# Optimization experiments

Hardware: AMD Instinct MI355X
Metric: run time of the kernel (lower is better)

Reference implementation:

```python
import jax, jax.numpy as jnp
import numpy as np

IN_FEATURES = 4096
OUT_FEATURES = 4096
BATCH = 4096
MASK_DENSITY = 0.05  # typical power-grid neighborhood sparsity


def setup_inputs() -> dict:
    key = jax.random.key(0)
    k_x, k_w, k_b, k_m = jax.random.split(key, 4)
    x = jax.random.normal(k_x, (BATCH, IN_FEATURES), dtype=jnp.float32)
    # kaiming_uniform_(a=sqrt(5)) -> uniform(-bound, bound), bound = sqrt(6/((1+5)*fan_in)) = 1/sqrt(fan_in)
    w_bound = 1.0 / np.sqrt(IN_FEATURES)
    weight = jax.random.uniform(k_w, (OUT_FEATURES, IN_FEATURES), dtype=jnp.float32,
                                minval=-w_bound, maxval=w_bound)
    bias = jax.random.uniform(k_b, (OUT_FEATURES,), dtype=jnp.float32,
                              minval=-w_bound, maxval=w_bound)
    # fixed binary neighborhood filter (non-trainable), int-valued {0,1} as in the torch module
    myFilter = (jax.random.uniform(k_m, (OUT_FEATURES, IN_FEATURES)) < MASK_DENSITY).astype(jnp.float32)
    return {"x": x, "weight": weight, "bias": bias, "myFilter": myFilter}


def reference(x, weight, bias, myFilter):
    # F.linear(input, weight * myFilter, bias): y = x @ (W * M)^T + b
    masked_w = weight * myFilter                      # [out, in]
    return jnp.einsum('bi,oi->bo', x, masked_w) + bias  # [batch, out]
```

## Files before the change

kernel.cpp:

```cpp
#include <hip/hip_runtime.h>
#include <hip/hip_bf16.h>
#include <stdint.h>

#define IN_F   4096
#define OUT_F  4096
#define BATCH  4096

typedef __bf16 bf16x8_t __attribute__((ext_vector_type(8)));
typedef float  f32x4_t  __attribute__((ext_vector_type(4)));

#define AS_GLOBAL(p) ((const __attribute__((address_space(1))) void*)(p))
#define AS_LDS(p)    ((__attribute__((address_space(3))) void*)(p))

__device__ __forceinline__ unsigned short f32_to_bf16_rne(float f) {
    union { float f; uint32_t u; } v; v.f = f;
    uint32_t u = v.u;
    u += 0x7FFFu + ((u >> 16) & 1u);
    return (unsigned short)(u >> 16);
}

__global__ __launch_bounds__(256)
void convert_kernel(const float* __restrict__ x,
                    const float* __restrict__ w,
                    const float* __restrict__ m,
                    unsigned short* __restrict__ xb,
                    unsigned short* __restrict__ wb) {
    const int64_t i = (int64_t)blockIdx.x * 256 + threadIdx.x;
    float4 xv = ((const float4*)x)[i];
    float4 wv = ((const float4*)w)[i];
    float4 mv = ((const float4*)m)[i];
    ushort4 xo, wo;
    xo.x = f32_to_bf16_rne(xv.x);
    xo.y = f32_to_bf16_rne(xv.y);
    xo.z = f32_to_bf16_rne(xv.z);
    xo.w = f32_to_bf16_rne(xv.w);
    wo.x = f32_to_bf16_rne(wv.x * mv.x);
    wo.y = f32_to_bf16_rne(wv.y * mv.y);
    wo.z = f32_to_bf16_rne(wv.z * mv.z);
    wo.w = f32_to_bf16_rne(wv.w * mv.w);
    ((ushort4*)xb)[i] = xo;
    ((ushort4*)wb)[i] = wo;
}

#define BM 128
#define BN 128
#define BK 64

__global__ __launch_bounds__(256)
void gemm_bt_bias_kernel(const unsigned short* __restrict__ A,
                         const unsigned short* __restrict__ B,
                         const float* __restrict__ bias,
                         float* __restrict__ C) {
    __shared__ __align__(16) unsigned short sA[BM * BK];
    __shared__ __align__(16) unsigned short sB[BN * BK];

    const int t    = threadIdx.x;
    const int wv   = t >> 6;
    const int lane = t & 63;
    const int quad = lane >> 4;
    const int l16  = lane & 15;

    const int bm = blockIdx.y * BM;
    const int bn = blockIdx.x * BN;

    const int wr = wv >> 1;
    const int wc = wv & 1;

    const int srow = t >> 3;
    const int scol = 8 * ((t & 7) ^ ((t >> 3) & 7));
    const unsigned short* gA = A + (int64_t)(bm + srow) * IN_F + scol;
    const unsigned short* gB = B + (int64_t)(bn + srow) * IN_F + scol;

    f32x4_t acc[4][4];
#pragma unroll
    for (int mi = 0; mi < 4; ++mi)
#pragma unroll
        for (int ni = 0; ni < 4; ++ni)
            acc[mi][ni] = (f32x4_t){0.f, 0.f, 0.f, 0.f};

    for (int k0 = 0; k0 < IN_F; k0 += BK) {
        __syncthreads();
#pragma unroll
        for (int r = 0; r < 4; ++r) {
            __builtin_amdgcn_global_load_lds(
                AS_GLOBAL(gA + (int64_t)r * 32 * IN_F + k0),
                AS_LDS((char*)sA + r * 4096 + wv * 1024 + (lane * 16)), 16, 0, 0);
            __builtin_amdgcn_global_load_lds(
                AS_GLOBAL(gB + (int64_t)r * 32 * IN_F + k0),
                AS_LDS((char*)sB + r * 4096 + wv * 1024 + (lane * 16)), 16, 0, 0);
        }
        __syncthreads();

#pragma unroll
        for (int ks = 0; ks < 2; ++ks) {
            bf16x8_t af[4], bf[4];
#pragma unroll
            for (int mi = 0; mi < 4; ++mi) {
                const int row = wr * 64 + mi * 16 + l16;
                const int ch  = (ks * 4 + quad) ^ (row & 7);
                af[mi] = *(const bf16x8_t*)(sA + row * BK + ch * 8);
            }
#pragma unroll
            for (int ni = 0; ni < 4; ++ni) {
                const int row = wc * 64 + ni * 16 + l16;
                const int ch  = (ks * 4 + quad) ^ (row & 7);
                bf[ni] = *(const bf16x8_t*)(sB + row * BK + ch * 8);
            }
#pragma unroll
            for (int mi = 0; mi < 4; ++mi)
#pragma unroll
                for (int ni = 0; ni < 4; ++ni)
                    acc[mi][ni] = __builtin_amdgcn_mfma_f32_16x16x32_bf16(
                        af[mi], bf[ni], acc[mi][ni], 0, 0, 0);
        }
    }

    float bv[4];
#pragma unroll
    for (int ni = 0; ni < 4; ++ni)
        bv[ni] = bias[bn + wc * 64 + ni * 16 + l16];

#pragma unroll
    for (int mi = 0; mi < 4; ++mi) {
        const int row0 = bm + wr * 64 + mi * 16 + quad * 4;
#pragma unroll
        for (int ni = 0; ni < 4; ++ni) {
            const int col = bn + wc * 64 + ni * 16 + l16;
#pragma unroll
            for (int reg = 0; reg < 4; ++reg)
                C[(int64_t)(row0 + reg) * OUT_F + col] = acc[mi][ni][reg] + bv[ni];
        }
    }
}

__global__ void fallback_gemm_kernel(const float* __restrict__ x,
                                     const float* __restrict__ w,
                                     const float* __restrict__ bias,
                                     const float* __restrict__ m,
                                     float* __restrict__ y) {
    __shared__ float sx[16][17];
    __shared__ float sw[16][17];
    const int tx = threadIdx.x, ty = threadIdx.y;
    const int row = blockIdx.y * 16 + ty;
    const int col = blockIdx.x * 16 + tx;
    float acc = 0.f;
    for (int k0 = 0; k0 < IN_F; k0 += 16) {
        sx[ty][tx] = x[(int64_t)row * IN_F + k0 + tx];
        const int64_t widx = (int64_t)(blockIdx.x * 16 + ty) * IN_F + k0 + tx;
        sw[ty][tx] = w[widx] * m[widx];
        __syncthreads();
#pragma unroll
        for (int kk = 0; kk < 16; ++kk)
            acc += sx[ty][kk] * sw[tx][kk];
        __syncthreads();
    }
    y[(int64_t)row * OUT_F + col] = acc + bias[col];
}

extern "C" void kernel_launch(void* const* d_in, const int* in_sizes, int n_in,
                              void* d_out, int out_size, void* d_ws, size_t ws_size,
                              hipStream_t stream) {
    const float* x    = (const float*)d_in[0];
    const float* w    = (const float*)d_in[1];
    const float* bias = (const float*)d_in[2];
    const float* m    = (const float*)d_in[3];
    float* y = (float*)d_out;

    const size_t need = (size_t)2 * (size_t)OUT_F * (size_t)IN_F * sizeof(unsigned short);

    if (ws_size >= need) {
        unsigned short* xb = (unsigned short*)d_ws;
        unsigned short* wb = xb + (size_t)BATCH * IN_F;

        convert_kernel<<<16384, 256, 0, stream>>>(x, w, m, xb, wb);

        dim3 grid(OUT_F / BN, BATCH / BM);
        gemm_bt_bias_kernel<<<grid, 256, 0, stream>>>(xb, wb, bias, y);
    } else {
        dim3 grid(OUT_F / 16, BATCH / 16);
        dim3 block(16, 16);
        fallback_gemm_kernel<<<grid, block, 0, stream>>>(x, w, bias, m, y);
    }
}
```

Before: 341.8 us.

## Enlarge GEMM tile to 256x128 and overlap next-tile loads with MFMA

The GEMM block tile grows from 128x128 to 256x128, so each wave now holds 8x4 accumulators, which raises data reuse per loaded B fragment. The main loop is restructured so the first k-half is computed, the second k-half fragments are read into registers, and then the next tile's global-to-LDS loads are issued before the second half's MFMAs run, overlapping load latency with compute. The convert kernel processes two vectors per thread with nontemporal loads and half the grid. Risks are higher register pressure (128 accumulator floats plus 12 fragments), lower occupancy, and a smaller grid of 512 blocks for 256 CUs.

```diff
diff --git a/kernel.cpp b/kernel.cpp
--- a/kernel.cpp
+++ b/kernel.cpp
@@ -8,6 +8,8 @@
 
 typedef __bf16 bf16x8_t __attribute__((ext_vector_type(8)));
 typedef float  f32x4_t  __attribute__((ext_vector_type(4)));
+typedef float  f32x4v   __attribute__((ext_vector_type(4)));
+typedef unsigned short u16x4v __attribute__((ext_vector_type(4)));
 
 #define AS_GLOBAL(p) ((const __attribute__((address_space(1))) void*)(p))
 #define AS_LDS(p)    ((__attribute__((address_space(3))) void*)(p))
@@ -25,24 +27,28 @@
                     const float* __restrict__ m,
                     unsigned short* __restrict__ xb,
                     unsigned short* __restrict__ wb) {
-    const int64_t i = (int64_t)blockIdx.x * 256 + threadIdx.x;
-    float4 xv = ((const float4*)x)[i];
-    float4 wv = ((const float4*)w)[i];
-    float4 mv = ((const float4*)m)[i];
-    ushort4 xo, wo;
-    xo.x = f32_to_bf16_rne(xv.x);
-    xo.y = f32_to_bf16_rne(xv.y);
-    xo.z = f32_to_bf16_rne(xv.z);
-    xo.w = f32_to_bf16_rne(xv.w);
-    wo.x = f32_to_bf16_rne(wv.x * mv.x);
-    wo.y = f32_to_bf16_rne(wv.y * mv.y);
-    wo.z = f32_to_bf16_rne(wv.z * mv.z);
-    wo.w = f32_to_bf16_rne(wv.w * mv.w);
-    ((ushort4*)xb)[i] = xo;
-    ((ushort4*)wb)[i] = wo;
-}
-
-#define BM 128
+    const int64_t i0 = (int64_t)blockIdx.x * 512 + threadIdx.x;
+#pragma unroll
+    for (int u = 0; u < 2; ++u) {
+        const int64_t i = i0 + u * 256;
+        f32x4v xv = __builtin_nontemporal_load(&((const f32x4v*)x)[i]);
+        f32x4v wv = __builtin_nontemporal_load(&((const f32x4v*)w)[i]);
+        f32x4v mv = __builtin_nontemporal_load(&((const f32x4v*)m)[i]);
+        u16x4v xo, wo;
+        xo.x = f32_to_bf16_rne(xv.x);
+        xo.y = f32_to_bf16_rne(xv.y);
+        xo.z = f32_to_bf16_rne(xv.z);
+        xo.w = f32_to_bf16_rne(xv.w);
+        wo.x = f32_to_bf16_rne(wv.x * mv.x);
+        wo.y = f32_to_bf16_rne(wv.y * mv.y);
+        wo.z = f32_to_bf16_rne(wv.z * mv.z);
+        wo.w = f32_to_bf16_rne(wv.w * mv.w);
+        ((u16x4v*)xb)[i] = xo;
+        ((u16x4v*)wb)[i] = wo;
+    }
+}
+
+#define BM 256
 #define BN 128
 #define BK 64
 
@@ -71,48 +77,71 @@
     const unsigned short* gA = A + (int64_t)(bm + srow) * IN_F + scol;
     const unsigned short* gB = B + (int64_t)(bn + srow) * IN_F + scol;
 
-    f32x4_t acc[4][4];
-#pragma unroll
-    for (int mi = 0; mi < 4; ++mi)
+#define ISSUE_TILE(k0)                                                        \
+    do {                                                                      \
+        _Pragma("unroll")                                                     \
+        for (int r = 0; r < 8; ++r)                                           \
+            __builtin_amdgcn_global_load_lds(                                 \
+                AS_GLOBAL(gA + (int64_t)r * 32 * IN_F + (k0)),                \
+                AS_LDS((char*)sA + r * 4096 + wv * 1024 + lane * 16), 16, 0, 0); \
+        _Pragma("unroll")                                                     \
+        for (int r = 0; r < 4; ++r)                                           \
+            __builtin_amdgcn_global_load_lds(                                 \
+                AS_GLOBAL(gB + (int64_t)r * 32 * IN_F + (k0)),                \
+                AS_LDS((char*)sB + r * 4096 + wv * 1024 + lane * 16), 16, 0, 0); \
+    } while (0)
+
+    f32x4_t acc[8][4];
+#pragma unroll
+    for (int mi = 0; mi < 8; ++mi)
 #pragma unroll
         for (int ni = 0; ni < 4; ++ni)
             acc[mi][ni] = (f32x4_t){0.f, 0.f, 0.f, 0.f};
 
+    ISSUE_TILE(0);
+
     for (int k0 = 0; k0 < IN_F; k0 += BK) {
         __syncthreads();
-#pragma unroll
-        for (int r = 0; r < 4; ++r) {
-            __builtin_amdgcn_global_load_lds(
-                AS_GLOBAL(gA + (int64_t)r * 32 * IN_F + k0),
-                AS_LDS((char*)sA + r * 4096 + wv * 1024 + (lane * 16)), 16, 0, 0);
-            __builtin_amdgcn_global_load_lds(
-                AS_GLOBAL(gB + (int64_t)r * 32 * IN_F + k0),
-                AS_LDS((char*)sB + r * 4096 + wv * 1024 + (lane * 16)), 16, 0, 0);
-        }
-        __syncthreads();
-
-#pragma unroll
-        for (int ks = 0; ks < 2; ++ks) {
-            bf16x8_t af[4], bf[4];
-#pragma unroll
-            for (int mi = 0; mi < 4; ++mi) {
-                const int row = wr * 64 + mi * 16 + l16;
-                const int ch  = (ks * 4 + quad) ^ (row & 7);
-                af[mi] = *(const bf16x8_t*)(sA + row * BK + ch * 8);
-            }
-#pragma unroll
-            for (int ni = 0; ni < 4; ++ni) {
-                const int row = wc * 64 + ni * 16 + l16;
-                const int ch  = (ks * 4 + quad) ^ (row & 7);
-                bf[ni] = *(const bf16x8_t*)(sB + row * BK + ch * 8);
-            }
-#pragma unroll
-            for (int mi = 0; mi < 4; ++mi)
-#pragma unroll
-                for (int ni = 0; ni < 4; ++ni)
-                    acc[mi][ni] = __builtin_amdgcn_mfma_f32_16x16x32_bf16(
-                        af[mi], bf[ni], acc[mi][ni], 0, 0, 0);
-        }
+
+        bf16x8_t bf0[4];
+#pragma unroll
+        for (int ni = 0; ni < 4; ++ni) {
+            const int row = wc * 64 + ni * 16 + l16;
+            bf0[ni] = *(const bf16x8_t*)(sB + row * BK + (quad ^ (row & 7)) * 8);
+        }
+#pragma unroll
+        for (int mi = 0; mi < 8; ++mi) {
+            const int row = wr * 128 + mi * 16 + l16;
+            bf16x8_t af = *(const bf16x8_t*)(sA + row * BK + (quad ^ (row & 7)) * 8);
+#pragma unroll
+            for (int ni = 0; ni < 4; ++ni)
+                acc[mi][ni] = __builtin_amdgcn_mfma_f32_16x16x32_bf16(
+                    af, bf0[ni], acc[mi][ni], 0, 0, 0);
+        }
+
+        bf16x8_t bf1[4], af1[8];
+#pragma unroll
+        for (int ni = 0; ni < 4; ++ni) {
+            const int row = wc * 64 + ni * 16 + l16;
+            bf1[ni] = *(const bf16x8_t*)(sB + row * BK + ((4 + quad) ^ (row & 7)) * 8);
+        }
+#pragma unroll
+        for (int mi = 0; mi < 8; ++mi) {
+            const int row = wr * 128 + mi * 16 + l16;
+            af1[mi] = *(const bf16x8_t*)(sA + row * BK + ((4 + quad) ^ (row & 7)) * 8);
+        }
+
+        __syncthreads();
+
+        if (k0 + BK < IN_F)
+            ISSUE_TILE(k0 + BK);
+
+#pragma unroll
+        for (int mi = 0; mi < 8; ++mi)
+#pragma unroll
+            for (int ni = 0; ni < 4; ++ni)
+                acc[mi][ni] = __builtin_amdgcn_mfma_f32_16x16x32_bf16(
+                    af1[mi], bf1[ni], acc[mi][ni], 0, 0, 0);
     }
 
     float bv[4];
@@ -121,8 +150,8 @@
         bv[ni] = bias[bn + wc * 64 + ni * 16 + l16];
 
 #pragma unroll
-    for (int mi = 0; mi < 4; ++mi) {
-        const int row0 = bm + wr * 64 + mi * 16 + quad * 4;
+    for (int mi = 0; mi < 8; ++mi) {
+        const int row0 = bm + wr * 128 + mi * 16 + quad * 4;
 #pragma unroll
         for (int ni = 0; ni < 4; ++ni) {
             const int col = bn + wc * 64 + ni * 16 + l16;
@@ -131,6 +160,7 @@
                 C[(int64_t)(row0 + reg) * OUT_F + col] = acc[mi][ni][reg] + bv[ni];
         }
     }
+#undef ISSUE_TILE
 }
 
 __global__ void fallback_gemm_kernel(const float* __restrict__ x,
@@ -172,7 +202,7 @@
         unsigned short* xb = (unsigned short*)d_ws;
         unsigned short* wb = xb + (size_t)BATCH * IN_F;
 
-        convert_kernel<<<16384, 256, 0, stream>>>(x, w, m, xb, wb);
+        convert_kernel<<<8192, 256, 0, stream>>>(x, w, m, xb, wb);
 
         dim3 grid(OUT_F / BN, BATCH / BM);
         gemm_bt_bias_kernel<<<grid, 256, 0, stream>>>(xb, wb, bias, y);
```

Result: slower. 384.1 us (+12.4%).

## Double-buffer GEMM LDS tiles and unroll nontemporal convert kernel

Applied to the files above, without the earlier changes.

The GEMM now keeps two LDS buffers per operand. It issues the direct global-to-LDS loads for the next K tile before computing on the current tile, which drops one barrier per iteration and aims to hide global load latency behind MFMA work. The convert kernel handles two float4 groups per thread with nontemporal loads and launches half as many blocks, to cut streaming overhead. This doubles LDS use per block, which can lower occupancy. The overlap also depends on the compiler not inserting a full vmcnt wait before the LDS reads.

```diff
diff --git a/kernel.cpp b/kernel.cpp
--- a/kernel.cpp
+++ b/kernel.cpp
@@ -8,6 +8,8 @@
 
 typedef __bf16 bf16x8_t __attribute__((ext_vector_type(8)));
 typedef float  f32x4_t  __attribute__((ext_vector_type(4)));
+typedef float  f32x4v   __attribute__((ext_vector_type(4)));
+typedef unsigned short u16x4v __attribute__((ext_vector_type(4)));
 
 #define AS_GLOBAL(p) ((const __attribute__((address_space(1))) void*)(p))
 #define AS_LDS(p)    ((__attribute__((address_space(3))) void*)(p))
@@ -25,21 +27,25 @@
                     const float* __restrict__ m,
                     unsigned short* __restrict__ xb,
                     unsigned short* __restrict__ wb) {
-    const int64_t i = (int64_t)blockIdx.x * 256 + threadIdx.x;
-    float4 xv = ((const float4*)x)[i];
-    float4 wv = ((const float4*)w)[i];
-    float4 mv = ((const float4*)m)[i];
-    ushort4 xo, wo;
-    xo.x = f32_to_bf16_rne(xv.x);
-    xo.y = f32_to_bf16_rne(xv.y);
-    xo.z = f32_to_bf16_rne(xv.z);
-    xo.w = f32_to_bf16_rne(xv.w);
-    wo.x = f32_to_bf16_rne(wv.x * mv.x);
-    wo.y = f32_to_bf16_rne(wv.y * mv.y);
-    wo.z = f32_to_bf16_rne(wv.z * mv.z);
-    wo.w = f32_to_bf16_rne(wv.w * mv.w);
-    ((ushort4*)xb)[i] = xo;
-    ((ushort4*)wb)[i] = wo;
+    const int64_t i0 = (int64_t)blockIdx.x * 512 + threadIdx.x;
+#pragma unroll
+    for (int u = 0; u < 2; ++u) {
+        const int64_t i = i0 + u * 256;
+        f32x4v xv = __builtin_nontemporal_load(&((const f32x4v*)x)[i]);
+        f32x4v wv = __builtin_nontemporal_load(&((const f32x4v*)w)[i]);
+        f32x4v mv = __builtin_nontemporal_load(&((const f32x4v*)m)[i]);
+        u16x4v xo, wo;
+        xo.x = f32_to_bf16_rne(xv.x);
+        xo.y = f32_to_bf16_rne(xv.y);
+        xo.z = f32_to_bf16_rne(xv.z);
+        xo.w = f32_to_bf16_rne(xv.w);
+        wo.x = f32_to_bf16_rne(wv.x * mv.x);
+        wo.y = f32_to_bf16_rne(wv.y * mv.y);
+        wo.z = f32_to_bf16_rne(wv.z * mv.z);
+        wo.w = f32_to_bf16_rne(wv.w * mv.w);
+        ((u16x4v*)xb)[i] = xo;
+        ((u16x4v*)wb)[i] = wo;
+    }
 }
 
 #define BM 128
@@ -51,8 +57,8 @@
                          const unsigned short* __restrict__ B,
                          const float* __restrict__ bias,
                          float* __restrict__ C) {
-    __shared__ __align__(16) unsigned short sA[BM * BK];
-    __shared__ __align__(16) unsigned short sB[BN * BK];
+    __shared__ __align__(16) unsigned short sA[2][BM * BK];
+    __shared__ __align__(16) unsigned short sB[2][BN * BK];
 
     const int t    = threadIdx.x;
     const int wv   = t >> 6;
@@ -71,6 +77,19 @@
     const unsigned short* gA = A + (int64_t)(bm + srow) * IN_F + scol;
     const unsigned short* gB = B + (int64_t)(bn + srow) * IN_F + scol;
 
+#define ISSUE_TILE(buf, k0)                                                   \
+    do {                                                                      \
+        _Pragma("unroll")                                                     \
+        for (int r = 0; r < 4; ++r) {                                         \
+            __builtin_amdgcn_global_load_lds(                                 \
+                AS_GLOBAL(gA + (int64_t)r * 32 * IN_F + (k0)),                \
+                AS_LDS((char*)sA[buf] + r * 4096 + wv * 1024 + lane * 16), 16, 0, 0); \
+            __builtin_amdgcn_global_load_lds(                                 \
+                AS_GLOBAL(gB + (int64_t)r * 32 * IN_F + (k0)),                \
+                AS_LDS((char*)sB[buf] + r * 4096 + wv * 1024 + lane * 16), 16, 0, 0); \
+        }                                                                     \
+    } while (0)
+
     f32x4_t acc[4][4];
 #pragma unroll
     for (int mi = 0; mi < 4; ++mi)
@@ -78,18 +97,17 @@
         for (int ni = 0; ni < 4; ++ni)
             acc[mi][ni] = (f32x4_t){0.f, 0.f, 0.f, 0.f};
 
-    for (int k0 = 0; k0 < IN_F; k0 += BK) {
+    ISSUE_TILE(0, 0);
+
+    int buf = 0;
+    for (int k0 = 0; k0 < IN_F; k0 += BK, buf ^= 1) {
         __syncthreads();
-#pragma unroll
-        for (int r = 0; r < 4; ++r) {
-            __builtin_amdgcn_global_load_lds(
-                AS_GLOBAL(gA + (int64_t)r * 32 * IN_F + k0),
-                AS_LDS((char*)sA + r * 4096 + wv * 1024 + (lane * 16)), 16, 0, 0);
-            __builtin_amdgcn_global_load_lds(
-                AS_GLOBAL(gB + (int64_t)r * 32 * IN_F + k0),
-                AS_LDS((char*)sB + r * 4096 + wv * 1024 + (lane * 16)), 16, 0, 0);
-        }
-        __syncthreads();
+
+        if (k0 + BK < IN_F)
+            ISSUE_TILE(buf ^ 1, k0 + BK);
+
+        const unsigned short* __restrict__ cA = sA[buf];
+        const unsigned short* __restrict__ cB = sB[buf];
 
 #pragma unroll
         for (int ks = 0; ks < 2; ++ks) {
@@ -98,13 +116,13 @@
             for (int mi = 0; mi < 4; ++mi) {
                 const int row = wr * 64 + mi * 16 + l16;
                 const int ch  = (ks * 4 + quad) ^ (row & 7);
-                af[mi] = *(const bf16x8_t*)(sA + row * BK + ch * 8);
+                af[mi] = *(const bf16x8_t*)(cA + row * BK + ch * 8);
             }
 #pragma unroll
             for (int ni = 0; ni < 4; ++ni) {
                 const int row = wc * 64 + ni * 16 + l16;
                 const int ch  = (ks * 4 + quad) ^ (row & 7);
-                bf[ni] = *(const bf16x8_t*)(sB + row * BK + ch * 8);
+                bf[ni] = *(const bf16x8_t*)(cB + row * BK + ch * 8);
             }
 #pragma unroll
             for (int mi = 0; mi < 4; ++mi)
@@ -131,6 +149,7 @@
                 C[(int64_t)(row0 + reg) * OUT_F + col] = acc[mi][ni][reg] + bv[ni];
         }
     }
+#undef ISSUE_TILE
 }
 
 __global__ void fallback_gemm_kernel(const float* __restrict__ x,
@@ -172,7 +191,7 @@
         unsigned short* xb = (unsigned short*)d_ws;
         unsigned short* wb = xb + (size_t)BATCH * IN_F;
 
-        convert_kernel<<<16384, 256, 0, stream>>>(x, w, m, xb, wb);
+        convert_kernel<<<8192, 256, 0, stream>>>(x, w, m, xb, wb);
 
         dim3 grid(OUT_F / BN, BATCH / BM);
         gemm_bt_bias_kernel<<<grid, 256, 0, stream>>>(xb, wb, bias, y);
```

New measurement: 324.7 us. -5.0%, faster.
